# Performance work log

Hardware: AMD Instinct MI355X
Metric: run time of the kernel (lower is better)

## Reference

```python
import jax, jax.numpy as jnp
import numpy as np

N = 199968   # active voxels (flat tokens)
W = 3125     # number of windows
S = 64       # window capacity
D = 128      # d_model
H = 8        # nhead
DH = D // H
DFF = 256


def layer_norm(x, g, b, eps=1e-5):
    m = x.mean(-1, keepdims=True)
    v = ((x - m) ** 2).mean(-1, keepdims=True)
    return (x - m) / jnp.sqrt(v + eps) * g + b


def setup_inputs() -> dict:
    key = jax.random.key(0)
    ks = jax.random.split(key, 12)
    s = 0.02
    src = jax.random.normal(ks[0], (N, D), dtype=jnp.float32)
    pos = jax.random.normal(ks[1], (W, S, D), dtype=jnp.float32)
    # token i occupies flat window-slot i; slots >= N are padding
    inds = jnp.arange(N, dtype=jnp.int64)
    key_padding_mask = (jnp.arange(W * S) >= N).reshape(W, S)  # True = pad
    in_proj_w = jax.random.normal(ks[2], (3 * D, D), dtype=jnp.float32) * s
    in_proj_b = jax.random.normal(ks[3], (3 * D,), dtype=jnp.float32) * s
    out_w = jax.random.normal(ks[4], (D, D), dtype=jnp.float32) * s
    out_b = jax.random.normal(ks[5], (D,), dtype=jnp.float32) * s
    w1 = jax.random.normal(ks[6], (DFF, D), dtype=jnp.float32) * s
    b1 = jax.random.normal(ks[7], (DFF,), dtype=jnp.float32) * s
    w2 = jax.random.normal(ks[8], (D, DFF), dtype=jnp.float32) * s
    b2 = jax.random.normal(ks[9], (D,), dtype=jnp.float32) * s
    ln1_g = jnp.ones((D,), jnp.float32); ln1_b = jnp.zeros((D,), jnp.float32)
    ln2_g = jnp.ones((D,), jnp.float32); ln2_b = jnp.zeros((D,), jnp.float32)
    return {"src": src, "pos": pos, "inds": inds,
            "key_padding_mask": key_padding_mask,
            "in_proj_w": in_proj_w, "in_proj_b": in_proj_b,
            "out_w": out_w, "out_b": out_b,
            "w1": w1, "b1": b1, "w2": w2, "b2": b2,
            "ln1_g": ln1_g, "ln1_b": ln1_b, "ln2_g": ln2_g, "ln2_b": ln2_b}


def reference(src, pos, inds, key_padding_mask, in_proj_w, in_proj_b,
              out_w, out_b, w1, b1, w2, b2, ln1_g, ln1_b, ln2_g, ln2_b):
    # ---- flat2window_v2: scatter flat tokens into window slots ----
    win = jnp.zeros((W * S, D), src.dtype).at[inds].set(src).reshape(W, S, D)
    # q = k = feat + pos, v = feat (post-norm, self-attention branch)
    qk_in = win + pos
    Wq, Wk, Wv = in_proj_w[:D], in_proj_w[D:2 * D], in_proj_w[2 * D:]
    bq, bk, bv = in_proj_b[:D], in_proj_b[D:2 * D], in_proj_b[2 * D:]
    q = (qk_in @ Wq.T + bq).reshape(W, S, H, DH)
    k = (qk_in @ Wk.T + bk).reshape(W, S, H, DH)
    v = (win @ Wv.T + bv).reshape(W, S, H, DH)
    scale = 1.0 / jnp.sqrt(jnp.asarray(DH, src.dtype))
    scores = jnp.einsum('wqhd,wkhd->whqk', q, k) * scale  # [W,H,S,S]
    scores = jnp.where(key_padding_mask[:, None, None, :], -jnp.inf, scores)
    attn = jax.nn.softmax(scores, axis=-1)
    o = jnp.einsum('whqk,wkhd->wqhd', attn, v).reshape(W, S, D)
    o = o @ out_w.T + out_b
    # ---- window2flat_v2: gather back to flat tokens ----
    att_out = o.reshape(W * S, D)[inds]
    # ---- residual + LN + FFN + LN (post_norm=True, dropout=0 eval) ----
    x = layer_norm(src + att_out, ln1_g, ln1_b)
    ffn = jax.nn.relu(x @ w1.T + b1) @ w2.T + b2
    x = layer_norm(x + ffn, ln2_g, ln2_b)
    return x
```

## Files before the change

### kernel.cpp

```cpp
#include <hip/hip_runtime.h>
#include <stdint.h>

typedef __attribute__((ext_vector_type(8))) short bf16x8;
typedef __attribute__((ext_vector_type(4))) float f32x4;
typedef __attribute__((ext_vector_type(16))) float f32x16;

#define MFMA16(a,b,c) __builtin_amdgcn_mfma_f32_16x16x32_bf16((a),(b),(c),0,0,0)
#define MFMA32(a,b,c) __builtin_amdgcn_mfma_f32_32x32x16_bf16((a),(b),(c),0,0,0)

#define RA 0
#define RB 16384
#define RC 32768
#define RED 49152
#define LDSB (49152 + 2048)
#define QSCALE 0.36067376022224085f

static __device__ __forceinline__ int swz16(int row, int byte){ return byte ^ ((row&15)<<4); }
static __device__ __forceinline__ int swz8 (int row, int byte){ return byte ^ ((row&7)<<4); }

static __device__ __forceinline__ void barrier_lds(){
  asm volatile("s_waitcnt lgkmcnt(0)" ::: "memory");
  __builtin_amdgcn_s_barrier();
  __builtin_amdgcn_sched_barrier(0);
}

static __device__ __forceinline__ uint32_t cvtpk(float lo, float hi){
  uint32_t r; asm("v_cvt_pk_bf16_f32 %0, %1, %2" : "=v"(r) : "v"(lo), "v"(hi)); return r;
}
static __device__ __forceinline__ unsigned short f2bf(float f){
  union { float f; uint32_t u; } c; c.f = f;
  return (unsigned short)((c.u + 0x7fffu + ((c.u >> 16) & 1u)) >> 16);
}
static __device__ __forceinline__ f32x16 zero16(){
  f32x16 z;
  #pragma unroll
  for (int e=0;e<16;++e) z[e]=0.f;
  return z;
}

static __device__ __forceinline__ void packPT(const f32x16 s, int hi, bf16x8& fA, bf16x8& fB){
  uint32_t PA0=cvtpk(s[0],s[1]),  PA1=cvtpk(s[2],s[3]);
  uint32_t PB0=cvtpk(s[4],s[5]),  PB1=cvtpk(s[6],s[7]);
  uint32_t PC0=cvtpk(s[8],s[9]),  PC1=cvtpk(s[10],s[11]);
  uint32_t PD0=cvtpk(s[12],s[13]),PD1=cvtpk(s[14],s[15]);
  uint32_t x0 = __shfl_xor(hi ? PA0 : PB0, 32);
  uint32_t x1 = __shfl_xor(hi ? PA1 : PB1, 32);
  uint32_t y0 = __shfl_xor(hi ? PC0 : PD0, 32);
  uint32_t y1 = __shfl_xor(hi ? PC1 : PD1, 32);
  union { uint32_t u[4]; bf16x8 v; } ua, ub;
  ua.u[0] = hi ? x0 : PA0;  ua.u[1] = hi ? x1 : PA1;
  ua.u[2] = hi ? PB0 : x0;  ua.u[3] = hi ? PB1 : x1;
  ub.u[0] = hi ? y0 : PC0;  ub.u[1] = hi ? y1 : PC1;
  ub.u[2] = hi ? PD0 : y0;  ub.u[3] = hi ? PD1 : y1;
  fA = ua.v; fB = ub.v;
}

__global__ void convert_weights(const float* __restrict__ ipw, const float* __restrict__ ow,
                                const float* __restrict__ w1, const float* __restrict__ w2,
                                const float* __restrict__ g1,
                                unsigned short* __restrict__ wsb){
  int i = blockIdx.x*256 + threadIdx.x;
  if (i >= 131072) return;
  const float* sp; int m, K, KC;
  bool isw1 = false;
  if (i < 49152)      { sp = ipw; m = i;         K=128; KC=4; }
  else if (i < 65536) { sp = ow;  m = i - 49152; K=128; KC=4; }
  else if (i < 98304) { sp = w1;  m = i - 65536; K=128; KC=4; isw1 = true; }
  else                { sp = w2;  m = i - 98304; K=256; KC=8; }
  int e  = m & 7;
  int L  = (m >> 3) & 63;
  int b  = m >> 9;
  int kc = b % KC;
  int Mt = b / KC;
  int d  = kc*32 + (L>>4)*8 + e;
  float v = sp[(Mt*16 + (L&15))*K + d];
  if (i < 16384) v *= QSCALE;
  if (isw1)      v *= g1[d];
  wsb[i] = f2bf(v);
}

__global__ void convert_aux(const float* __restrict__ w1, const float* __restrict__ b1,
                            const float* __restrict__ g1, const float* __restrict__ be1,
                            float* __restrict__ auxp){
  int f = threadIdx.x;
  float s_be = 0.f, s_g = 0.f;
  for (int d=0; d<128; ++d){
    float w = w1[f*128+d];
    s_be += w * be1[d];
    s_g  += w * g1[d];
  }
  auxp[f]       = b1[f] + s_be;
  auxp[256 + f] = s_g;
}

__global__ __launch_bounds__(256, 3) void enc_kernel(
    const float* __restrict__ src, const float* __restrict__ pos,
    const float* __restrict__ ipb, const float* __restrict__ obp,
    const float* __restrict__ b2p,
    const float* __restrict__ g1p, const float* __restrict__ be1p,
    const float* __restrict__ g2p, const float* __restrict__ be2p,
    const unsigned short* __restrict__ wb,
    float* __restrict__ out, int nTok)
{
  __shared__ __align__(16) char sm[LDSB];
  const int win  = blockIdx.x;
  const int tid  = threadIdx.x;
  const int lane = tid & 63;
  const int wid  = tid >> 6;
  const int l15  = lane & 15;
  const int lg   = lane >> 4;
  const int l31  = lane & 31;
  const int hi   = lane >> 5;
  const f32x4 FZ = {0.f,0.f,0.f,0.f};
  const int colbase = wid*32;
  const unsigned short* wlane = wb + lane*8;
  const float* auxp = (const float*)(wb + 131072);
  const int valid = nTok - win*64;

  f32x4 srcv[2][4];
  #pragma unroll
  for (int Mtl=0;Mtl<2;++Mtl){
    #pragma unroll
    for (int g=0;g<4;++g){
      int row  = g*16 + l15;
      int grow = win*64 + row;
      int col  = colbase + Mtl*16 + lg*4;
      f32x4 sv = FZ;
      if (grow < nTok) sv = *(const f32x4*)(src + (size_t)grow*128 + col);
      f32x4 pv = *(const f32x4*)(pos + (size_t)win*8192 + row*128 + col);
      srcv[Mtl][g] = sv;
      uint2 wv, qv;
      wv.x = cvtpk(sv[0], sv[1]);             wv.y = cvtpk(sv[2], sv[3]);
      qv.x = cvtpk(sv[0]+pv[0], sv[1]+pv[1]); qv.y = cvtpk(sv[2]+pv[2], sv[3]+pv[3]);
      int cb = col*2;
      *(uint2*)(sm + RA + row*256 + swz16(row, cb)) = qv;
      *(uint2*)(sm + RB + row*256 + swz16(row, cb)) = wv;
    }
  }
  barrier_lds();

  {
    {
      bf16x8 wv8[8];
      #pragma unroll
      for (int i=0;i<8;++i)
        wv8[i] = *(const bf16x8*)(wlane + (size_t)(((16 + wid*2 + (i>>2))*4 + (i&3)) << 9));
      f32x4 vacc[2][4];
      #pragma unroll
      for (int Mtl=0;Mtl<2;++Mtl){
        #pragma unroll
        for (int g=0;g<4;++g) vacc[Mtl][g] = FZ;
      }
      #pragma unroll
      for (int kc=0;kc<4;++kc){
        bf16x8 bw[4];
        #pragma unroll
        for (int g=0;g<4;++g){
          int r2 = g*16 + l15;
          bw[g] = *(const bf16x8*)(sm + RB + r2*256 + swz16(r2, kc*64 + lg*16));
        }
        #pragma unroll
        for (int Mtl=0;Mtl<2;++Mtl){
          #pragma unroll
          for (int g=0;g<4;++g) vacc[Mtl][g] = MFMA16(wv8[Mtl*4+kc], bw[g], vacc[Mtl][g]);
        }
      }
      #pragma unroll
      for (int Mtl=0;Mtl<2;++Mtl){
        f32x4 b4 = *(const f32x4*)(ipb + 256 + colbase + Mtl*16 + lg*4);
        #pragma unroll
        for (int g=0;g<4;++g){
          #pragma unroll
          for (int r=0;r<4;++r){
            int d = colbase + Mtl*16 + lg*4 + r, tok = g*16 + l15;
            *(unsigned short*)(sm + RC + d*128 + swz8(d, tok*2)) = f2bf(vacc[Mtl][g][r] + b4[r]);
          }
        }
      }
    }

    f32x4 qacc[2][4];
    {
      bf16x8 wq8[8];
      #pragma unroll
      for (int i=0;i<8;++i)
        wq8[i] = *(const bf16x8*)(wlane + (size_t)((( 0 + wid*2 + (i>>2))*4 + (i&3)) << 9));
      #pragma unroll
      for (int Mtl=0;Mtl<2;++Mtl){
        #pragma unroll
        for (int g=0;g<4;++g) qacc[Mtl][g]=FZ;
      }
      #pragma unroll
      for (int kc=0;kc<4;++kc){
        bf16x8 bq[4];
        #pragma unroll
        for (int g=0;g<4;++g){
          int r2 = g*16 + l15;
          bq[g] = *(const bf16x8*)(sm + RA + r2*256 + swz16(r2, kc*64 + lg*16));
        }
        #pragma unroll
        for (int Mtl=0;Mtl<2;++Mtl){
          #pragma unroll
          for (int g=0;g<4;++g) qacc[Mtl][g] = MFMA16(wq8[Mtl*4+kc], bq[g], qacc[Mtl][g]);
        }
      }
    }
    barrier_lds();

    #pragma unroll
    for (int Mtl=0;Mtl<2;++Mtl){
      f32x4 qb4 = *(const f32x4*)(ipb + colbase + Mtl*16 + lg*4);
      #pragma unroll
      for (int g=0;g<4;++g){
        int tok = g*16 + l15;
        int cb  = (colbase + Mtl*16 + lg*4)*2;
        uint2 qp;
        qp.x = cvtpk(qacc[Mtl][g][0]+qb4[0]*QSCALE, qacc[Mtl][g][1]+qb4[1]*QSCALE);
        qp.y = cvtpk(qacc[Mtl][g][2]+qb4[2]*QSCALE, qacc[Mtl][g][3]+qb4[3]*QSCALE);
        *(uint2*)(sm + RB + tok*256 + swz16(tok, cb)) = qp;
      }
    }

    f32x4 kacc[2][4];
    {
      bf16x8 wk8[8];
      #pragma unroll
      for (int i=0;i<8;++i)
        wk8[i] = *(const bf16x8*)(wlane + (size_t)((( 8 + wid*2 + (i>>2))*4 + (i&3)) << 9));
      #pragma unroll
      for (int Mtl=0;Mtl<2;++Mtl){
        #pragma unroll
        for (int g=0;g<4;++g) kacc[Mtl][g]=FZ;
      }
      #pragma unroll
      for (int kc=0;kc<4;++kc){
        bf16x8 bq[4];
        #pragma unroll
        for (int g=0;g<4;++g){
          int r2 = g*16 + l15;
          bq[g] = *(const bf16x8*)(sm + RA + r2*256 + swz16(r2, kc*64 + lg*16));
        }
        #pragma unroll
        for (int Mtl=0;Mtl<2;++Mtl){
          #pragma unroll
          for (int g=0;g<4;++g) kacc[Mtl][g] = MFMA16(wk8[Mtl*4+kc], bq[g], kacc[Mtl][g]);
        }
      }
    }
    barrier_lds();

    #pragma unroll
    for (int Mtl=0;Mtl<2;++Mtl){
      f32x4 kb4 = *(const f32x4*)(ipb + 128 + colbase + Mtl*16 + lg*4);
      #pragma unroll
      for (int g=0;g<4;++g){
        int tok = g*16 + l15;
        int cb  = (colbase + Mtl*16 + lg*4)*2;
        uint2 kp;
        kp.x = cvtpk(kacc[Mtl][g][0]+kb4[0], kacc[Mtl][g][1]+kb4[1]);
        kp.y = cvtpk(kacc[Mtl][g][2]+kb4[2], kacc[Mtl][g][3]+kb4[3]);
        *(uint2*)(sm + RA + tok*256 + swz16(tok, cb)) = kp;
      }
    }
  }

  #pragma unroll
  for (int hh=0; hh<2; ++hh){
    const int head = wid*2 + hh;
    bf16x8 ka0 = *(const bf16x8*)(sm + RA + (     l31)*256 + swz16(l31,    head*32 + hi*16));
    bf16x8 ka1 = *(const bf16x8*)(sm + RA + (32 + l31)*256 + swz16(32+l31, head*32 + hi*16));
    #pragma unroll
    for (int qt=0; qt<2; ++qt){
      int qrow = qt*32 + l31;
      bf16x8 qb = *(const bf16x8*)(sm + RB + qrow*256 + swz16(qrow, head*32 + hi*16));
      f32x16 s0 = MFMA32(ka0, qb, zero16());
      f32x16 s1 = MFMA32(ka1, qb, zero16());
      if (valid < 64){
        #pragma unroll
        for (int e=0;e<16;++e){
          int kk = (e&3) + 8*(e>>2) + 4*hi;
          if (kk      >= valid) s0[e] = -1e30f;
          if (kk + 32 >= valid) s1[e] = -1e30f;
        }
      }
      #pragma unroll
      for (int e=0;e<16;++e) s0[e] = __builtin_amdgcn_exp2f(s0[e]);
      #pragma unroll
      for (int e=0;e<16;++e) s1[e] = __builtin_amdgcn_exp2f(s1[e]);
      float t[8];
      #pragma unroll
      for (int e=0;e<8;++e) t[e] = (s0[2*e]+s0[2*e+1]) + (s1[2*e]+s1[2*e+1]);
      float u0 = t[0]+t[1], u1 = t[2]+t[3], u2 = t[4]+t[5], u3 = t[6]+t[7];
      float sum = (u0+u1)+(u2+u3);
      sum += __shfl_xor(sum, 32);
      float rden = __builtin_amdgcn_rcpf(sum);

      bf16x8 fr[4];
      packPT(s0, hi, fr[0], fr[1]);
      packPT(s1, hi, fr[2], fr[3]);
      f32x16 oacc = zero16();
      #pragma unroll
      for (int kc=0;kc<4;++kc){
        int vrow = head*16 + l15;
        bf16x8 va = *(const bf16x8*)(sm + RC + vrow*128 + swz8(vrow, kc*32 + hi*16));
        oacc = MFMA32(va, fr[kc], oacc);
      }
      int tok = qt*32 + l31;
      uint2 o01, o23;
      o01.x = cvtpk(oacc[0]*rden, oacc[1]*rden);
      o01.y = cvtpk(oacc[2]*rden, oacc[3]*rden);
      o23.x = cvtpk(oacc[4]*rden, oacc[5]*rden);
      o23.y = cvtpk(oacc[6]*rden, oacc[7]*rden);
      *(uint2*)(sm + RB + tok*256 + swz16(tok, (head*16 + 4*hi)*2))     = o01;
      *(uint2*)(sm + RB + tok*256 + swz16(tok, (head*16 + 8 + 4*hi)*2)) = o23;
    }
  }
  barrier_lds();

  f32x4 xva[2][4];
  float mean4[4], rstd4[4];
  {
    bf16x8 wo8[8];
    #pragma unroll
    for (int i=0;i<8;++i)
      wo8[i] = *(const bf16x8*)(wlane + 49152 + (size_t)(((wid*2 + (i>>2))*4 + (i&3)) << 9));
    f32x4 oa[2][4];
    #pragma unroll
    for (int Mtl=0;Mtl<2;++Mtl){
      #pragma unroll
      for (int g=0;g<4;++g) oa[Mtl][g] = FZ;
    }
    #pragma unroll
    for (int kc=0;kc<4;++kc){
      bf16x8 bo[4];
      #pragma unroll
      for (int g=0;g<4;++g){
        int r2 = g*16 + l15;
        bo[g] = *(const bf16x8*)(sm + RB + r2*256 + swz16(r2, kc*64 + lg*16));
      }
      #pragma unroll
      for (int Mtl=0;Mtl<2;++Mtl){
        #pragma unroll
        for (int g=0;g<4;++g) oa[Mtl][g] = MFMA16(wo8[Mtl*4+kc], bo[g], oa[Mtl][g]);
      }
    }
    #pragma unroll
    for (int Mtl=0;Mtl<2;++Mtl){
      f32x4 ob4 = *(const f32x4*)(obp + colbase + Mtl*16 + lg*4);
      #pragma unroll
      for (int g=0;g<4;++g){
        #pragma unroll
        for (int r=0;r<4;++r) xva[Mtl][g][r] = oa[Mtl][g][r] + ob4[r] + srcv[Mtl][g][r];
      }
    }
    float* redc = (float*)(sm + RED);
    #pragma unroll
    for (int g=0;g<4;++g){
      float ts=0.f, tq=0.f;
      #pragma unroll
      for (int Mtl=0;Mtl<2;++Mtl){
        #pragma unroll
        for (int r=0;r<4;++r){ float v = xva[Mtl][g][r]; ts += v; tq += v*v; }
      }
      ts += __shfl_xor(ts,16); tq += __shfl_xor(tq,16);
      ts += __shfl_xor(ts,32); tq += __shfl_xor(tq,32);
      if (lg == 0) *(float2*)(redc + (g*16+l15)*8 + wid*2) = make_float2(ts, tq);
    }
    #pragma unroll
    for (int Mtl=0;Mtl<2;++Mtl){
      #pragma unroll
      for (int g=0;g<4;++g){
        int tok = g*16 + l15;
        int cb  = (colbase + Mtl*16 + lg*4)*2;
        uint2 xp;
        xp.x = cvtpk(xva[Mtl][g][0], xva[Mtl][g][1]);
        xp.y = cvtpk(xva[Mtl][g][2], xva[Mtl][g][3]);
        *(uint2*)(sm + RA + tok*256 + swz16(tok, cb)) = xp;
      }
    }
    barrier_lds();

    #pragma unroll
    for (int g=0;g<4;++g){
      int tok = g*16 + l15;
      f32x4 ra = *(const f32x4*)(redc + tok*8);
      f32x4 rb = *(const f32x4*)(redc + tok*8 + 4);
      float sum = ra[0]+ra[2]+rb[0]+rb[2];
      float sq  = ra[1]+ra[3]+rb[1]+rb[3];
      mean4[g] = sum*(1.f/128.f);
      rstd4[g] = __builtin_amdgcn_rsqf(sq*(1.f/128.f) - mean4[g]*mean4[g] + 1e-5f);
    }
    #pragma unroll
    for (int Mtl=0;Mtl<2;++Mtl){
      f32x4 g4 = *(const f32x4*)(g1p  + colbase + Mtl*16 + lg*4);
      f32x4 e4 = *(const f32x4*)(be1p + colbase + Mtl*16 + lg*4);
      #pragma unroll
      for (int g=0;g<4;++g){
        #pragma unroll
        for (int r=0;r<4;++r) xva[Mtl][g][r] = (xva[Mtl][g][r]-mean4[g])*rstd4[g]*g4[r] + e4[r];
      }
    }
  }

  {
    char* hreg = (wid < 2) ? (sm + RB) : (sm + RC);
    int   hoff = (wid & 1)*64;
    #pragma unroll 1
    for (int half=0; half<2; ++half){
      bf16x8 wf[8];
      #pragma unroll
      for (int i=0;i<8;++i)
        wf[i] = *(const bf16x8*)(wlane + 65536 + (size_t)(((wid*4 + half*2 + (i>>2))*4 + (i&3)) << 9));
      f32x4 ha[2][4];
      #pragma unroll
      for (int Mtl=0;Mtl<2;++Mtl){
        #pragma unroll
        for (int g=0;g<4;++g) ha[Mtl][g] = FZ;
      }
      #pragma unroll
      for (int kc=0;kc<4;++kc){
        bf16x8 bx[4];
        #pragma unroll
        for (int g=0;g<4;++g){
          int r2 = g*16 + l15;
          bx[g] = *(const bf16x8*)(sm + RA + r2*256 + swz16(r2, kc*64 + lg*16));
        }
        #pragma unroll
        for (int Mtl=0;Mtl<2;++Mtl){
          #pragma unroll
          for (int g=0;g<4;++g) ha[Mtl][g] = MFMA16(wf[Mtl*4+kc], bx[g], ha[Mtl][g]);
        }
      }
      #pragma unroll
      for (int Mtl=0;Mtl<2;++Mtl){
        int Mg = half*2 + Mtl;
        f32x4 b1f4 = *(const f32x4*)(auxp +       wid*64 + Mg*16 + lg*4);
        f32x4 rs14 = *(const f32x4*)(auxp + 256 + wid*64 + Mg*16 + lg*4);
        #pragma unroll
        for (int g=0;g<4;++g){
          int tok = g*16 + l15;
          float rr = rstd4[g], cm = rstd4[g]*mean4[g];
          float h0 = fmaxf(rr*ha[Mtl][g][0] - cm*rs14[0] + b1f4[0], 0.f);
          float h1 = fmaxf(rr*ha[Mtl][g][1] - cm*rs14[1] + b1f4[1], 0.f);
          float h2 = fmaxf(rr*ha[Mtl][g][2] - cm*rs14[2] + b1f4[2], 0.f);
          float h3 = fmaxf(rr*ha[Mtl][g][3] - cm*rs14[3] + b1f4[3], 0.f);
          int cb = (hoff + Mg*16 + lg*4)*2;
          uint2 hp;
          hp.x = cvtpk(h0, h1);
          hp.y = cvtpk(h2, h3);
          *(uint2*)(hreg + tok*256 + swz16(tok, cb)) = hp;
        }
      }
    }
  }
  barrier_lds();

  {
    f32x4 fa[2][4];
    #pragma unroll
    for (int Mtl=0;Mtl<2;++Mtl){
      #pragma unroll
      for (int g=0;g<4;++g) fa[Mtl][g] = FZ;
    }
    #pragma unroll 1
    for (int half=0; half<2; ++half){
      bf16x8 wg[8];
      #pragma unroll
      for (int i=0;i<8;++i)
        wg[i] = *(const bf16x8*)(wlane + 98304 + (size_t)(((wid*2 + (i>>2))*8 + half*4 + (i&3)) << 9));
      const char* hsrc = sm + (half ? RC : RB);
      #pragma unroll
      for (int kc=0;kc<4;++kc){
        bf16x8 bh[4];
        #pragma unroll
        for (int g=0;g<4;++g){
          int r2 = g*16 + l15;
          bh[g] = *(const bf16x8*)(hsrc + r2*256 + swz16(r2, kc*64 + lg*16));
        }
        #pragma unroll
        for (int Mtl=0;Mtl<2;++Mtl){
          #pragma unroll
          for (int g=0;g<4;++g) fa[Mtl][g] = MFMA16(wg[Mtl*4+kc], bh[g], fa[Mtl][g]);
        }
      }
    }
    #pragma unroll
    for (int Mtl=0;Mtl<2;++Mtl){
      f32x4 b24 = *(const f32x4*)(b2p + colbase + Mtl*16 + lg*4);
      #pragma unroll
      for (int g=0;g<4;++g){
        #pragma unroll
        for (int r=0;r<4;++r) fa[Mtl][g][r] += b24[r] + xva[Mtl][g][r];
      }
    }
    float* redc = (float*)(sm + RED);
    #pragma unroll
    for (int g=0;g<4;++g){
      float ts=0.f, tq=0.f;
      #pragma unroll
      for (int Mtl=0;Mtl<2;++Mtl){
        #pragma unroll
        for (int r=0;r<4;++r){ float v = fa[Mtl][g][r]; ts += v; tq += v*v; }
      }
      ts += __shfl_xor(ts,16); tq += __shfl_xor(tq,16);
      ts += __shfl_xor(ts,32); tq += __shfl_xor(tq,32);
      if (lg == 0) *(float2*)(redc + (g*16+l15)*8 + wid*2) = make_float2(ts, tq);
    }
    barrier_lds();
    float m2[4], r2v[4];
    #pragma unroll
    for (int g=0;g<4;++g){
      int tok = g*16 + l15;
      f32x4 ra = *(const f32x4*)(redc + tok*8);
      f32x4 rb = *(const f32x4*)(redc + tok*8 + 4);
      float sum = ra[0]+ra[2]+rb[0]+rb[2];
      float sq  = ra[1]+ra[3]+rb[1]+rb[3];
      m2[g]  = sum*(1.f/128.f);
      r2v[g] = __builtin_amdgcn_rsqf(sq*(1.f/128.f) - m2[g]*m2[g] + 1e-5f);
    }
    #pragma unroll
    for (int Mtl=0;Mtl<2;++Mtl){
      f32x4 g4 = *(const f32x4*)(g2p  + colbase + Mtl*16 + lg*4);
      f32x4 e4 = *(const f32x4*)(be2p + colbase + Mtl*16 + lg*4);
      #pragma unroll
      for (int g=0;g<4;++g){
        int tok = g*16 + l15;
        f32x4 o4;
        #pragma unroll
        for (int r=0;r<4;++r) o4[r] = (fa[Mtl][g][r]-m2[g])*r2v[g]*g4[r] + e4[r];
        int X = ((colbase + Mtl*16 + lg*4)*4) ^ (l15<<4);
        *(f32x4*)(sm + ((tok<32)? RA : RB) + (tok&31)*512 + X) = o4;
      }
    }
    barrier_lds();
    #pragma unroll
    for (int j=0;j<8;++j){
      int row  = wid*16 + j*2 + hi;
      int grow = win*64 + row;
      if (grow < nTok){
        int X = (l31*16) ^ ((row&15)<<4);
        f32x4 v = *(const f32x4*)(sm + ((row<32)? RA : RB) + (row&31)*512 + X);
        *(f32x4*)(out + (size_t)grow*128 + l31*4) = v;
      }
    }
  }
}

extern "C" void kernel_launch(void* const* d_in, const int* in_sizes, int n_in,
                              void* d_out, int out_size, void* d_ws, size_t ws_size,
                              hipStream_t stream) {
  const float* src = (const float*)d_in[0];
  const float* pos = (const float*)d_in[1];
  const float* ipw = (const float*)d_in[4];
  const float* ipb = (const float*)d_in[5];
  const float* ow  = (const float*)d_in[6];
  const float* ob  = (const float*)d_in[7];
  const float* w1  = (const float*)d_in[8];
  const float* b1  = (const float*)d_in[9];
  const float* w2  = (const float*)d_in[10];
  const float* b2  = (const float*)d_in[11];
  const float* g1  = (const float*)d_in[12];
  const float* be1 = (const float*)d_in[13];
  const float* g2  = (const float*)d_in[14];
  const float* be2 = (const float*)d_in[15];
  int nTok = in_sizes[0] / 128;
  int nWin = in_sizes[1] / 8192;
  unsigned short* wsb = (unsigned short*)d_ws;
  float* auxp = (float*)(wsb + 131072);

  hipLaunchKernelGGL(convert_weights, dim3(512), dim3(256), 0, stream, ipw, ow, w1, w2, g1, wsb);
  hipLaunchKernelGGL(convert_aux, dim3(1), dim3(256), 0, stream, w1, b1, g1, be1, auxp);
  hipLaunchKernelGGL(enc_kernel, dim3(nWin), dim3(256), 0, stream,
                     src, pos, ipb, ob, b2, g1, be1, g2, be2, wsb,
                     (float*)d_out, nTok);
}
```

Before: 158.6 us.

## Drop LN1 folding into W1, prefetch weights before barriers, transpose V MFMA

Stops folding the LN1 gamma/beta and mean/rstd algebra into the W1 weights, which removes the convert_aux launch and applies LN1 explicitly before writing x to LDS. The output-projection, first FFN and second FFN weight fragments are now loaded from global memory before the preceding barriers so their latency overlaps the sync. The V projection swaps its MFMA operands so each lane writes packed 4-token bf16 vectors instead of scalar shorts. The sched_barrier after each LDS barrier is removed. The trade is higher register pressure from the prefetched fragments, plus LN1 becoming extra per-element work inside the main kernel.

```diff
diff --git a/kernel.cpp b/kernel.cpp
--- a/kernel.cpp
+++ b/kernel.cpp
@@ -21,7 +21,6 @@
 static __device__ __forceinline__ void barrier_lds(){
   asm volatile("s_waitcnt lgkmcnt(0)" ::: "memory");
   __builtin_amdgcn_s_barrier();
-  __builtin_amdgcn_sched_barrier(0);
 }
 
 static __device__ __forceinline__ uint32_t cvtpk(float lo, float hi){
@@ -57,46 +56,28 @@
 
 __global__ void convert_weights(const float* __restrict__ ipw, const float* __restrict__ ow,
                                 const float* __restrict__ w1, const float* __restrict__ w2,
-                                const float* __restrict__ g1,
                                 unsigned short* __restrict__ wsb){
   int i = blockIdx.x*256 + threadIdx.x;
   if (i >= 131072) return;
   const float* sp; int m, K, KC;
-  bool isw1 = false;
   if (i < 49152)      { sp = ipw; m = i;         K=128; KC=4; }
   else if (i < 65536) { sp = ow;  m = i - 49152; K=128; KC=4; }
-  else if (i < 98304) { sp = w1;  m = i - 65536; K=128; KC=4; isw1 = true; }
+  else if (i < 98304) { sp = w1;  m = i - 65536; K=128; KC=4; }
   else                { sp = w2;  m = i - 98304; K=256; KC=8; }
   int e  = m & 7;
   int L  = (m >> 3) & 63;
   int b  = m >> 9;
   int kc = b % KC;
   int Mt = b / KC;
-  int d  = kc*32 + (L>>4)*8 + e;
-  float v = sp[(Mt*16 + (L&15))*K + d];
+  float v = sp[(Mt*16 + (L&15))*K + kc*32 + (L>>4)*8 + e];
   if (i < 16384) v *= QSCALE;
-  if (isw1)      v *= g1[d];
   wsb[i] = f2bf(v);
-}
-
-__global__ void convert_aux(const float* __restrict__ w1, const float* __restrict__ b1,
-                            const float* __restrict__ g1, const float* __restrict__ be1,
-                            float* __restrict__ auxp){
-  int f = threadIdx.x;
-  float s_be = 0.f, s_g = 0.f;
-  for (int d=0; d<128; ++d){
-    float w = w1[f*128+d];
-    s_be += w * be1[d];
-    s_g  += w * g1[d];
-  }
-  auxp[f]       = b1[f] + s_be;
-  auxp[256 + f] = s_g;
 }
 
 __global__ __launch_bounds__(256, 3) void enc_kernel(
     const float* __restrict__ src, const float* __restrict__ pos,
     const float* __restrict__ ipb, const float* __restrict__ obp,
-    const float* __restrict__ b2p,
+    const float* __restrict__ b1p, const float* __restrict__ b2p,
     const float* __restrict__ g1p, const float* __restrict__ be1p,
     const float* __restrict__ g2p, const float* __restrict__ be2p,
     const unsigned short* __restrict__ wb,
@@ -114,7 +95,6 @@
   const f32x4 FZ = {0.f,0.f,0.f,0.f};
   const int colbase = wid*32;
   const unsigned short* wlane = wb + lane*8;
-  const float* auxp = (const float*)(wb + 131072);
   const int valid = nTok - win*64;
 
   f32x4 srcv[2][4];
@@ -153,28 +133,28 @@
       }
       #pragma unroll
       for (int kc=0;kc<4;++kc){
-        bf16x8 bw[4];
+        bf16x8 aw[4];
         #pragma unroll
         for (int g=0;g<4;++g){
           int r2 = g*16 + l15;
-          bw[g] = *(const bf16x8*)(sm + RB + r2*256 + swz16(r2, kc*64 + lg*16));
+          aw[g] = *(const bf16x8*)(sm + RB + r2*256 + swz16(r2, kc*64 + lg*16));
         }
         #pragma unroll
         for (int Mtl=0;Mtl<2;++Mtl){
           #pragma unroll
-          for (int g=0;g<4;++g) vacc[Mtl][g] = MFMA16(wv8[Mtl*4+kc], bw[g], vacc[Mtl][g]);
-        }
-      }
-      #pragma unroll
-      for (int Mtl=0;Mtl<2;++Mtl){
-        f32x4 b4 = *(const f32x4*)(ipb + 256 + colbase + Mtl*16 + lg*4);
-        #pragma unroll
-        for (int g=0;g<4;++g){
-          #pragma unroll
-          for (int r=0;r<4;++r){
-            int d = colbase + Mtl*16 + lg*4 + r, tok = g*16 + l15;
-            *(unsigned short*)(sm + RC + d*128 + swz8(d, tok*2)) = f2bf(vacc[Mtl][g][r] + b4[r]);
-          }
+          for (int g=0;g<4;++g) vacc[Mtl][g] = MFMA16(aw[g], wv8[Mtl*4+kc], vacc[Mtl][g]);
+        }
+      }
+      #pragma unroll
+      for (int Mtl=0;Mtl<2;++Mtl){
+        int d = colbase + Mtl*16 + l15;
+        float bv = ipb[256 + d];
+        #pragma unroll
+        for (int g=0;g<4;++g){
+          uint2 vp;
+          vp.x = cvtpk(vacc[Mtl][g][0]+bv, vacc[Mtl][g][1]+bv);
+          vp.y = cvtpk(vacc[Mtl][g][2]+bv, vacc[Mtl][g][3]+bv);
+          *(uint2*)(sm + RC + d*128 + swz8(d, (g*16 + lg*4)*2)) = vp;
         }
       }
     }
@@ -315,15 +295,14 @@
       *(uint2*)(sm + RB + tok*256 + swz16(tok, (head*16 + 8 + 4*hi)*2)) = o23;
     }
   }
+  bf16x8 wo8[8];
+  #pragma unroll
+  for (int i=0;i<8;++i)
+    wo8[i] = *(const bf16x8*)(wlane + 49152 + (size_t)(((wid*2 + (i>>2))*4 + (i&3)) << 9));
   barrier_lds();
 
   f32x4 xva[2][4];
-  float mean4[4], rstd4[4];
   {
-    bf16x8 wo8[8];
-    #pragma unroll
-    for (int i=0;i<8;++i)
-      wo8[i] = *(const bf16x8*)(wlane + 49152 + (size_t)(((wid*2 + (i>>2))*4 + (i&3)) << 9));
     f32x4 oa[2][4];
     #pragma unroll
     for (int Mtl=0;Mtl<2;++Mtl){
@@ -366,20 +345,8 @@
       ts += __shfl_xor(ts,32); tq += __shfl_xor(tq,32);
       if (lg == 0) *(float2*)(redc + (g*16+l15)*8 + wid*2) = make_float2(ts, tq);
     }
-    #pragma unroll
-    for (int Mtl=0;Mtl<2;++Mtl){
-      #pragma unroll
-      for (int g=0;g<4;++g){
-        int tok = g*16 + l15;
-        int cb  = (colbase + Mtl*16 + lg*4)*2;
-        uint2 xp;
-        xp.x = cvtpk(xva[Mtl][g][0], xva[Mtl][g][1]);
-        xp.y = cvtpk(xva[Mtl][g][2], xva[Mtl][g][3]);
-        *(uint2*)(sm + RA + tok*256 + swz16(tok, cb)) = xp;
-      }
-    }
     barrier_lds();
-
+    float mean4[4], rstd4[4];
     #pragma unroll
     for (int g=0;g<4;++g){
       int tok = g*16 + l15;
@@ -396,11 +363,22 @@
       f32x4 e4 = *(const f32x4*)(be1p + colbase + Mtl*16 + lg*4);
       #pragma unroll
       for (int g=0;g<4;++g){
+        int tok = g*16 + l15;
+        int cb  = (colbase + Mtl*16 + lg*4)*2;
         #pragma unroll
         for (int r=0;r<4;++r) xva[Mtl][g][r] = (xva[Mtl][g][r]-mean4[g])*rstd4[g]*g4[r] + e4[r];
+        uint2 xp;
+        xp.x = cvtpk(xva[Mtl][g][0], xva[Mtl][g][1]);
+        xp.y = cvtpk(xva[Mtl][g][2], xva[Mtl][g][3]);
+        *(uint2*)(sm + RA + tok*256 + swz16(tok, cb)) = xp;
       }
     }
   }
+  bf16x8 wf0[8];
+  #pragma unroll
+  for (int i=0;i<8;++i)
+    wf0[i] = *(const bf16x8*)(wlane + 65536 + (size_t)(((wid*4 + (i>>2))*4 + (i&3)) << 9));
+  barrier_lds();
 
   {
     char* hreg = (wid < 2) ? (sm + RB) : (sm + RC);
@@ -410,7 +388,8 @@
       bf16x8 wf[8];
       #pragma unroll
       for (int i=0;i<8;++i)
-        wf[i] = *(const bf16x8*)(wlane + 65536 + (size_t)(((wid*4 + half*2 + (i>>2))*4 + (i&3)) << 9));
+        wf[i] = half ? *(const bf16x8*)(wlane + 65536 + (size_t)(((wid*4 + 2 + (i>>2))*4 + (i&3)) << 9))
+                     : wf0[i];
       f32x4 ha[2][4];
       #pragma unroll
       for (int Mtl=0;Mtl<2;++Mtl){
@@ -434,16 +413,14 @@
       #pragma unroll
       for (int Mtl=0;Mtl<2;++Mtl){
         int Mg = half*2 + Mtl;
-        f32x4 b1f4 = *(const f32x4*)(auxp +       wid*64 + Mg*16 + lg*4);
-        f32x4 rs14 = *(const f32x4*)(auxp + 256 + wid*64 + Mg*16 + lg*4);
+        f32x4 b14 = *(const f32x4*)(b1p + wid*64 + Mg*16 + lg*4);
         #pragma unroll
         for (int g=0;g<4;++g){
           int tok = g*16 + l15;
-          float rr = rstd4[g], cm = rstd4[g]*mean4[g];
-          float h0 = fmaxf(rr*ha[Mtl][g][0] - cm*rs14[0] + b1f4[0], 0.f);
-          float h1 = fmaxf(rr*ha[Mtl][g][1] - cm*rs14[1] + b1f4[1], 0.f);
-          float h2 = fmaxf(rr*ha[Mtl][g][2] - cm*rs14[2] + b1f4[2], 0.f);
-          float h3 = fmaxf(rr*ha[Mtl][g][3] - cm*rs14[3] + b1f4[3], 0.f);
+          float h0 = fmaxf(ha[Mtl][g][0]+b14[0], 0.f);
+          float h1 = fmaxf(ha[Mtl][g][1]+b14[1], 0.f);
+          float h2 = fmaxf(ha[Mtl][g][2]+b14[2], 0.f);
+          float h3 = fmaxf(ha[Mtl][g][3]+b14[3], 0.f);
           int cb = (hoff + Mg*16 + lg*4)*2;
           uint2 hp;
           hp.x = cvtpk(h0, h1);
@@ -453,6 +430,10 @@
       }
     }
   }
+  bf16x8 wg0[8];
+  #pragma unroll
+  for (int i=0;i<8;++i)
+    wg0[i] = *(const bf16x8*)(wlane + 98304 + (size_t)(((wid*2 + (i>>2))*8 + (i&3)) << 9));
   barrier_lds();
 
   {
@@ -467,7 +448,8 @@
       bf16x8 wg[8];
       #pragma unroll
       for (int i=0;i<8;++i)
-        wg[i] = *(const bf16x8*)(wlane + 98304 + (size_t)(((wid*2 + (i>>2))*8 + half*4 + (i&3)) << 9));
+        wg[i] = half ? *(const bf16x8*)(wlane + 98304 + (size_t)(((wid*2 + (i>>2))*8 + 4 + (i&3)) << 9))
+                     : wg0[i];
       const char* hsrc = sm + (half ? RC : RB);
       #pragma unroll
       for (int kc=0;kc<4;++kc){
@@ -566,11 +548,9 @@
   int nTok = in_sizes[0] / 128;
   int nWin = in_sizes[1] / 8192;
   unsigned short* wsb = (unsigned short*)d_ws;
-  float* auxp = (float*)(wsb + 131072);
-
-  hipLaunchKernelGGL(convert_weights, dim3(512), dim3(256), 0, stream, ipw, ow, w1, w2, g1, wsb);
-  hipLaunchKernelGGL(convert_aux, dim3(1), dim3(256), 0, stream, w1, b1, g1, be1, auxp);
+
+  hipLaunchKernelGGL(convert_weights, dim3(512), dim3(256), 0, stream, ipw, ow, w1, w2, wsb);
   hipLaunchKernelGGL(enc_kernel, dim3(nWin), dim3(256), 0, stream,
-                     src, pos, ipb, ob, b2, g1, be1, g2, be2, wsb,
+                     src, pos, ipb, ob, b1, b2, g1, be1, g2, be2, wsb,
                      (float*)d_out, nTok);
 }
```

Result: slower. 166.2 us (+4.8%).
